# Kernel optimization log

Measured on AMD Instinct MI355X. Metric: run time of the kernel, lower is better.

## Reference

```python
import jax, jax.numpy as jnp
import numpy as np

K = 2  # shift stride from module init


def setup_inputs() -> dict:
    key = jax.random.key(0)
    k1, k2, k3 = jax.random.split(key, 3)
    # x: [B, C, D, H, W] dense volumetric features
    x = jax.random.normal(k1, (2, 128, 48, 48, 48), dtype=jnp.float32)
    # 1x1x1 Conv3d weight [out_channels, 2*in_channels] (kernel dims squeezed) + bias
    W = jax.random.normal(k2, (128, 256), dtype=jnp.float32) * 0.02
    b = jax.random.normal(k3, (128,), dtype=jnp.float32) * 0.02
    return {"x": x, "W": W, "b": b}


def _max_relative(x):
    # torch.cat([x[..., -i:], x[..., :-i]], dim=ax) == roll by +i along ax
    B, C, D, H, Wd = x.shape
    xj = jnp.zeros_like(x)  # x - x
    for axis, n in ((2, D), (3, H), (4, Wd)):
        for i in range(K, n, K):  # static shift schedule, fine under jit
            xj = jnp.maximum(xj, x - jnp.roll(x, i, axis=axis))
    return xj


def reference(x, W, b):
    xj = _max_relative(x)
    y = jnp.concatenate([x, xj], axis=1)  # [B, 2C, D, H, W]
    # 1x1x1 conv == channel GEMM
    out = jnp.einsum('bcdhw,oc->bodhw', y, W) + b[None, :, None, None, None]
    return jax.nn.relu(out)
```

## Files before the change

### kernel.cpp

```cpp
#include <hip/hip_runtime.h>
#include <hip/hip_bf16.h>

#define SVOL 110592
#define HD   2304
#define NDIM 48

typedef __attribute__((ext_vector_type(4))) float f32x4;
typedef __attribute__((ext_vector_type(8))) short bf16x8;
typedef __attribute__((ext_vector_type(2))) unsigned int u32x2;
typedef unsigned short ushort_t;
typedef unsigned int uint_t;

__global__ __launch_bounds__(256) void wconv_kernel(const float* __restrict__ W,
                                                    ushort_t* __restrict__ Wb) {
    int i = blockIdx.x * 256 + threadIdx.x;
    float f = W[i];
    __hip_bfloat16 h = __float2bfloat16(f);
    Wb[i] = *(ushort_t*)&h;
}

__global__ __launch_bounds__(256) void tables_kernel(const float* __restrict__ x,
                                                     float* __restrict__ tabDp,
                                                     float* __restrict__ tabH,
                                                     float* __restrict__ tabW) {
    __shared__ __align__(16) float sl[4 * HD];
    const int bc   = blockIdx.x;
    const int part = blockIdx.y;
    const float* __restrict__ xp = x + (size_t)bc * SVOL + (size_t)part * 16 * HD;
    const int t    = threadIdx.x;
    const int w4   = t >> 6;
    const int lane = t & 63;
    const int dlh  = t / NDIM;
    const int wh   = t - dlh * NDIM;

    f32x4 accD[3][2];
    #pragma unroll
    for (int s = 0; s < 3; ++s)
        #pragma unroll
        for (int p = 0; p < 2; ++p)
            #pragma unroll
            for (int e = 0; e < 4; ++e) accD[s][p][e] = 3e38f;

    for (int q = 0; q < 4; ++q) {
        const float* __restrict__ qp = xp + (size_t)q * 4 * HD;
        #pragma unroll
        for (int k = 0; k < 9; ++k) {
            const int i16 = (k * 4 + w4) * 64 + lane;
            __builtin_amdgcn_global_load_lds(
                (const __attribute__((address_space(1))) void*)(qp + (size_t)i16 * 4),
                (__attribute__((address_space(3))) void*)&sl[(k * 4 + w4) * 256],
                16, 0, 0);
        }
        __syncthreads();

        #pragma unroll
        for (int s = 0; s < 3; ++s) {
            const int j = t + s * 256;
            if (j < 576) {
                #pragma unroll
                for (int dl = 0; dl < 4; ++dl) {
                    f32x4 v = ((const f32x4*)sl)[dl * 576 + j];
                    #pragma unroll
                    for (int e = 0; e < 4; ++e)
                        accD[s][dl & 1][e] = fminf(accD[s][dl & 1][e], v[e]);
                }
            }
        }
        if (t < 192) {
            const int d = part * 16 + q * 4 + dlh;
            {
                const float* pb = sl + dlh * HD + wh;
                float m0 = 3e38f, m1 = 3e38f;
                #pragma unroll
                for (int h = 0; h < NDIM; h += 2) {
                    m0 = fminf(m0, pb[h * NDIM]);
                    m1 = fminf(m1, pb[(h + 1) * NDIM]);
                }
                tabH[(size_t)bc * 2 * HD + d * NDIM + wh]      = m0;
                tabH[(size_t)bc * 2 * HD + HD + d * NDIM + wh] = m1;
            }
            {
                const f32x4* pr = (const f32x4*)(sl + dlh * HD + wh * NDIM);
                const int rot = wh % 12;
                float m0 = 3e38f, m1 = 3e38f;
                #pragma unroll
                for (int j = 0; j < 12; ++j) {
                    int jj = j + rot; if (jj >= 12) jj -= 12;
                    f32x4 v = pr[jj];
                    m0 = fminf(m0, fminf(v[0], v[2]));
                    m1 = fminf(m1, fminf(v[1], v[3]));
                }
                tabW[(size_t)bc * 2 * HD + d * NDIM + wh]      = m0;
                tabW[(size_t)bc * 2 * HD + HD + d * NDIM + wh] = m1;
            }
        }
        __syncthreads();
    }

    float* tDo = tabDp + ((size_t)part * 256 + bc) * 2 * HD;
    #pragma unroll
    for (int s = 0; s < 3; ++s) {
        const int j = t + s * 256;
        if (j < 576) {
            *((f32x4*)(tDo + j * 4))      = accD[s][0];
            *((f32x4*)(tDo + HD + j * 4)) = accD[s][1];
        }
    }
}

__global__ __launch_bounds__(256) void elem_kernel(const float* __restrict__ x,
                                                   const float* __restrict__ tabDp,
                                                   const float* __restrict__ tabH,
                                                   const float* __restrict__ tabW,
                                                   ushort_t* __restrict__ ybf) {
    __shared__ __align__(16) float sD[2 * HD];
    __shared__ __align__(16) float sH[2 * 384];
    __shared__ __align__(16) float sW[2 * 384];
    const int slab = blockIdx.x;
    const int bc   = blockIdx.y;
    const int t    = threadIdx.x;
    const int b = bc >> 7, c = bc & 127;

    const float* tD0 = tabDp + ((size_t)0 * 256 + bc) * 2 * HD;
    const float* tD1 = tabDp + ((size_t)1 * 256 + bc) * 2 * HD;
    const float* tD2 = tabDp + ((size_t)2 * 256 + bc) * 2 * HD;
    for (int i = t; i < 2 * HD / 4; i += 256) {
        f32x4 a = ((const f32x4*)tD0)[i];
        f32x4 d1 = ((const f32x4*)tD1)[i];
        f32x4 d2 = ((const f32x4*)tD2)[i];
        f32x4 m;
        #pragma unroll
        for (int j = 0; j < 4; ++j) m[j] = fminf(a[j], fminf(d1[j], d2[j]));
        ((f32x4*)sD)[i] = m;
    }
    const float* tH = tabH + (size_t)bc * 2 * HD;
    const float* tW = tabW + (size_t)bc * 2 * HD;
    for (int i = t; i < 96; i += 256) {
        ((f32x4*)sH)[i]      = ((const f32x4*)(tH + slab * 384))[i];
        ((f32x4*)sH)[96 + i] = ((const f32x4*)(tH + HD + slab * 384))[i];
        ((f32x4*)sW)[i]      = ((const f32x4*)(tW + slab * 384))[i];
        ((f32x4*)sW)[96 + i] = ((const f32x4*)(tW + HD + slab * 384))[i];
    }
    __syncthreads();

    const float* __restrict__ xp = x + (size_t)bc * SVOL + (size_t)slab * 8 * HD;
    ushort_t* yx = ybf + (size_t)(b * 256 + c) * SVOL + (size_t)slab * 8 * HD;
    ushort_t* yj = yx + (size_t)128 * SVOL;

    for (int i4 = t; i4 < 8 * HD / 4; i4 += 256) {
        const int s = i4 * 4;
        const int dl = s / HD;
        const int r  = s - dl * HD;
        const int h  = r / NDIM;
        const int w0 = r - h * NDIM;
        const int pd = dl & 1, ph = h & 1;

        f32x4 v  = *(const f32x4*)(xp + s);
        f32x4 mD = *(const f32x4*)(sD + pd * HD + r);
        f32x4 mH = *(const f32x4*)(sH + ph * 384 + dl * NDIM + w0);
        const float mW0 = sW[dl * NDIM + h];
        const float mW1 = sW[384 + dl * NDIM + h];

        union { __hip_bfloat16 h4[4]; uint2 u; } ox, oj;
        #pragma unroll
        for (int j = 0; j < 4; ++j) {
            const float mm  = fminf(mD[j], fminf(mH[j], (j & 1) ? mW1 : mW0));
            const float xjv = fmaxf(0.0f, v[j] - mm);
            ox.h4[j] = __float2bfloat16(v[j]);
            oj.h4[j] = __float2bfloat16(xjv);
        }
        *(uint2*)(yx + s) = ox.u;
        *(uint2*)(yj + s) = oj.u;
    }
}

#define TPB 4
__global__ __launch_bounds__(256, 2) void gemm_kernel(const ushort_t* __restrict__ ybf,
                                                      const ushort_t* __restrict__ Wb,
                                                      const float* __restrict__ bias,
                                                      float* __restrict__ out) {
    __shared__ __align__(1024) ushort_t ytile[2][16384];
    const int tile0 = blockIdx.x * TPB;
    const int b  = blockIdx.y;
    const int t  = threadIdx.x;
    const int wid = t >> 6, lane = t & 63;
    const ushort_t* __restrict__ yb = ybf + (size_t)b * 256 * SVOL;

    const int wm = wid;
    const int l15 = lane & 15, l4 = lane >> 4;

    const ushort_t* wp = Wb + (size_t)(wm * 32 + l15) * 256 + l4 * 8;
    bf16x8 aw[2][8];
    #pragma unroll
    for (int m = 0; m < 2; ++m)
        #pragma unroll
        for (int kk = 0; kk < 8; ++kk)
            aw[m][kk] = *(const bf16x8*)(wp + ((size_t)m * 16 * 256 + kk * 32));
    float bv[2];
    #pragma unroll
    for (int m = 0; m < 2; ++m) bv[m] = bias[wm * 32 + m * 16 + l15];

    const int g    = lane >> 5;
    const int l5   = lane & 31;
    const int sq   = l5 >> 3;
    const int row  = (l5 >> 1) & 3;
    const int colh = l5 & 1;

#define STAGE(buf, tile)                                                              \
    {                                                                                 \
        const int s0_ = (tile) * 64;                                                  \
        _Pragma("unroll")                                                             \
        for (int it = 0; it < 8; ++it) {                                              \
            const int cq0 = (it * 4 + wid) * 2;                                       \
            const int c   = (cq0 + g) * 4 + row;                                      \
            const ushort_t* src = yb + (size_t)c * SVOL + (s0_ + sq * 16 + colh * 8); \
            __builtin_amdgcn_global_load_lds(                                         \
                (const __attribute__((address_space(1))) void*)src,                   \
                (__attribute__((address_space(3))) void*)&ytile[buf][cq0 * 256],      \
                16, 0, 0);                                                            \
        }                                                                             \
    }

    const uint_t lds_base = (uint_t)(uintptr_t)(__attribute__((address_space(3))) ushort_t*)&ytile[0][0];
    const uint_t addr0 = lds_base + (uint_t)(l4 * 1024 + l15 * 8);
    float* ob = out + (size_t)b * 128 * SVOL;

    STAGE(0, tile0)

    #pragma unroll
    for (int tt = 0; tt < TPB; ++tt) {
        __builtin_amdgcn_s_barrier();
        if (tt + 1 < TPB) STAGE((tt + 1) & 1, tile0 + tt + 1)
        __builtin_amdgcn_sched_barrier(0);
        if (tt == 0 || tt + 1 == TPB) asm volatile("s_waitcnt vmcnt(8)" ::: "memory");
        else                          asm volatile("s_waitcnt vmcnt(16)" ::: "memory");
        __builtin_amdgcn_sched_barrier(0);
        __builtin_amdgcn_s_barrier();

        const uint_t addrB = addr0 + (uint_t)((tt & 1) * 32768);
        f32x4 acc[4][2] = {};
        #pragma unroll
        for (int ph = 0; ph < 2; ++ph) {
            u32x2 lo[4][4], hi[4][4];
            #pragma unroll
            for (int kk = 0; kk < 4; ++kk)
                #pragma unroll
                for (int n = 0; n < 4; ++n) {
                    const uint_t ad = addrB + (uint_t)((ph * 4 + kk) * 4096 + n * 128);
                    asm volatile("ds_read_b64_tr_b16 %0, %2 offset:0\n\t"
                                 "ds_read_b64_tr_b16 %1, %2 offset:512"
                                 : "=&v"(lo[kk][n]), "=&v"(hi[kk][n]) : "v"(ad) : "memory");
                }
            asm volatile("s_waitcnt lgkmcnt(0)" ::: "memory");
            __builtin_amdgcn_sched_barrier(0);
            #pragma unroll
            for (int kk = 0; kk < 4; ++kk)
                #pragma unroll
                for (int n = 0; n < 4; ++n) {
                    union { u32x2 u2[2]; bf16x8 v; } cvt;
                    cvt.u2[0] = lo[kk][n]; cvt.u2[1] = hi[kk][n];
                    #pragma unroll
                    for (int m = 0; m < 2; ++m)
                        acc[n][m] = __builtin_amdgcn_mfma_f32_16x16x32_bf16(cvt.v, aw[m][ph * 4 + kk], acc[n][m], 0, 0, 0);
                }
        }

        const int s_b = (tile0 + tt) * 64;
        #pragma unroll
        for (int n = 0; n < 4; ++n)
            #pragma unroll
            for (int m = 0; m < 2; ++m) {
                const int o = wm * 32 + m * 16 + l15;
                const int s = s_b + n * 16 + l4 * 4;
                f32x4 r;
                #pragma unroll
                for (int j = 0; j < 4; ++j) r[j] = fmaxf(acc[n][m][j] + bv[m], 0.0f);
                *(f32x4*)(ob + (size_t)o * SVOL + s) = r;
            }
    }
#undef STAGE
}

extern "C" void kernel_launch(void* const* d_in, const int* in_sizes, int n_in,
                              void* d_out, int out_size, void* d_ws, size_t ws_size,
                              hipStream_t stream) {
    const float* x    = (const float*)d_in[0];
    const float* W    = (const float*)d_in[1];
    const float* bias = (const float*)d_in[2];
    float* out = (float*)d_out;

    ushort_t* ybf = (ushort_t*)d_ws;
    ushort_t* Wb  = (ushort_t*)((char*)d_ws + (size_t)2 * 256 * SVOL * 2);

    float* tabDp = (float*)d_out;
    float* tabH  = tabDp + (size_t)3 * 256 * 2 * HD;
    float* tabW  = tabH  + (size_t)256 * 2 * HD;

    wconv_kernel<<<128, 256, 0, stream>>>(W, Wb);
    tables_kernel<<<dim3(256, 3), 256, 0, stream>>>(x, tabDp, tabH, tabW);
    elem_kernel<<<dim3(6, 256), 256, 0, stream>>>(x, tabDp, tabH, tabW, ybf);
    gemm_kernel<<<dim3(SVOL / 64 / TPB, 2), 256, 0, stream>>>(ybf, Wb, bias, out);
}
```

Baseline: 137.4 us.

## Fuse elementwise relative-max construction into GEMM staging, drop bf16 intermediate

Removes the elem_kernel, which wrote a full bf16 copy of the concatenated [x, xj] tensor to global memory, and instead computes x and xj per tile inside the GEMM, packing them into registers and storing to LDS. A small merge kernel collapses the three partial D tables into one so the GEMM reads a single table. Weights are now reloaded from global memory per k-step instead of kept resident in registers, which frees registers but adds global/L2 traffic. The async global-to-LDS pipeline is replaced with register prefetch plus two __syncthreads per tile, which may expose more load latency.

```diff
diff --git a/kernel.cpp b/kernel.cpp
--- a/kernel.cpp
+++ b/kernel.cpp
@@ -108,74 +108,23 @@
     }
 }
 
-__global__ __launch_bounds__(256) void elem_kernel(const float* __restrict__ x,
-                                                   const float* __restrict__ tabDp,
-                                                   const float* __restrict__ tabH,
-                                                   const float* __restrict__ tabW,
-                                                   ushort_t* __restrict__ ybf) {
-    __shared__ __align__(16) float sD[2 * HD];
-    __shared__ __align__(16) float sH[2 * 384];
-    __shared__ __align__(16) float sW[2 * 384];
-    const int slab = blockIdx.x;
-    const int bc   = blockIdx.y;
-    const int t    = threadIdx.x;
-    const int b = bc >> 7, c = bc & 127;
-
-    const float* tD0 = tabDp + ((size_t)0 * 256 + bc) * 2 * HD;
-    const float* tD1 = tabDp + ((size_t)1 * 256 + bc) * 2 * HD;
-    const float* tD2 = tabDp + ((size_t)2 * 256 + bc) * 2 * HD;
-    for (int i = t; i < 2 * HD / 4; i += 256) {
-        f32x4 a = ((const f32x4*)tD0)[i];
-        f32x4 d1 = ((const f32x4*)tD1)[i];
-        f32x4 d2 = ((const f32x4*)tD2)[i];
-        f32x4 m;
-        #pragma unroll
-        for (int j = 0; j < 4; ++j) m[j] = fminf(a[j], fminf(d1[j], d2[j]));
-        ((f32x4*)sD)[i] = m;
-    }
-    const float* tH = tabH + (size_t)bc * 2 * HD;
-    const float* tW = tabW + (size_t)bc * 2 * HD;
-    for (int i = t; i < 96; i += 256) {
-        ((f32x4*)sH)[i]      = ((const f32x4*)(tH + slab * 384))[i];
-        ((f32x4*)sH)[96 + i] = ((const f32x4*)(tH + HD + slab * 384))[i];
-        ((f32x4*)sW)[i]      = ((const f32x4*)(tW + slab * 384))[i];
-        ((f32x4*)sW)[96 + i] = ((const f32x4*)(tW + HD + slab * 384))[i];
-    }
-    __syncthreads();
-
-    const float* __restrict__ xp = x + (size_t)bc * SVOL + (size_t)slab * 8 * HD;
-    ushort_t* yx = ybf + (size_t)(b * 256 + c) * SVOL + (size_t)slab * 8 * HD;
-    ushort_t* yj = yx + (size_t)128 * SVOL;
-
-    for (int i4 = t; i4 < 8 * HD / 4; i4 += 256) {
-        const int s = i4 * 4;
-        const int dl = s / HD;
-        const int r  = s - dl * HD;
-        const int h  = r / NDIM;
-        const int w0 = r - h * NDIM;
-        const int pd = dl & 1, ph = h & 1;
-
-        f32x4 v  = *(const f32x4*)(xp + s);
-        f32x4 mD = *(const f32x4*)(sD + pd * HD + r);
-        f32x4 mH = *(const f32x4*)(sH + ph * 384 + dl * NDIM + w0);
-        const float mW0 = sW[dl * NDIM + h];
-        const float mW1 = sW[384 + dl * NDIM + h];
-
-        union { __hip_bfloat16 h4[4]; uint2 u; } ox, oj;
-        #pragma unroll
-        for (int j = 0; j < 4; ++j) {
-            const float mm  = fminf(mD[j], fminf(mH[j], (j & 1) ? mW1 : mW0));
-            const float xjv = fmaxf(0.0f, v[j] - mm);
-            ox.h4[j] = __float2bfloat16(v[j]);
-            oj.h4[j] = __float2bfloat16(xjv);
-        }
-        *(uint2*)(yx + s) = ox.u;
-        *(uint2*)(yj + s) = oj.u;
-    }
+__global__ __launch_bounds__(256) void merge_kernel(const float* __restrict__ tabDp,
+                                                    float* __restrict__ tabD) {
+    const int i = blockIdx.x * 256 + threadIdx.x;
+    f32x4 a  = ((const f32x4*)tabDp)[i];
+    f32x4 d1 = ((const f32x4*)(tabDp + (size_t)256 * 2 * HD))[i];
+    f32x4 d2 = ((const f32x4*)(tabDp + (size_t)2 * 256 * 2 * HD))[i];
+    f32x4 m;
+    #pragma unroll
+    for (int j = 0; j < 4; ++j) m[j] = fminf(a[j], fminf(d1[j], d2[j]));
+    ((f32x4*)tabD)[i] = m;
 }
 
 #define TPB 4
-__global__ __launch_bounds__(256, 2) void gemm_kernel(const ushort_t* __restrict__ ybf,
+__global__ __launch_bounds__(256, 2) void gemm_kernel(const float* __restrict__ x,
+                                                      const float* __restrict__ tabD,
+                                                      const float* __restrict__ tabH,
+                                                      const float* __restrict__ tabW,
                                                       const ushort_t* __restrict__ Wb,
                                                       const float* __restrict__ bias,
                                                       float* __restrict__ out) {
@@ -184,69 +133,82 @@
     const int b  = blockIdx.y;
     const int t  = threadIdx.x;
     const int wid = t >> 6, lane = t & 63;
-    const ushort_t* __restrict__ yb = ybf + (size_t)b * 256 * SVOL;
-
-    const int wm = wid;
+    const int row  = lane & 3;
+    const int colq = (lane >> 2) & 3;
+    const int sqq  = (lane >> 4) & 3;
+    const int sloc = (sqq * 4 + colq) * 4;
     const int l15 = lane & 15, l4 = lane >> 4;
 
-    const ushort_t* wp = Wb + (size_t)(wm * 32 + l15) * 256 + l4 * 8;
-    bf16x8 aw[2][8];
-    #pragma unroll
-    for (int m = 0; m < 2; ++m)
-        #pragma unroll
-        for (int kk = 0; kk < 8; ++kk)
-            aw[m][kk] = *(const bf16x8*)(wp + ((size_t)m * 16 * 256 + kk * 32));
+    const float* __restrict__ xb = x + (size_t)b * 128 * SVOL;
+    const size_t tbb = (size_t)b * 128 * 2 * HD;
+
+    const ushort_t* wp = Wb + (size_t)(wid * 32 + l15) * 256 + l4 * 8;
     float bv[2];
     #pragma unroll
-    for (int m = 0; m < 2; ++m) bv[m] = bias[wm * 32 + m * 16 + l15];
-
-    const int g    = lane >> 5;
-    const int l5   = lane & 31;
-    const int sq   = l5 >> 3;
-    const int row  = (l5 >> 1) & 3;
-    const int colh = l5 & 1;
-
-#define STAGE(buf, tile)                                                              \
-    {                                                                                 \
-        const int s0_ = (tile) * 64;                                                  \
-        _Pragma("unroll")                                                             \
-        for (int it = 0; it < 8; ++it) {                                              \
-            const int cq0 = (it * 4 + wid) * 2;                                       \
-            const int c   = (cq0 + g) * 4 + row;                                      \
-            const ushort_t* src = yb + (size_t)c * SVOL + (s0_ + sq * 16 + colh * 8); \
-            __builtin_amdgcn_global_load_lds(                                         \
-                (const __attribute__((address_space(1))) void*)src,                   \
-                (__attribute__((address_space(3))) void*)&ytile[buf][cq0 * 256],      \
-                16, 0, 0);                                                            \
-        }                                                                             \
-    }
+    for (int m = 0; m < 2; ++m) bv[m] = bias[wid * 32 + m * 16 + l15];
+
+    const int d  = (tile0 * 64) / HD;
+    const int rb = tile0 * 64 - d * HD;
+    const int pd = d & 1;
+
+    uint2 pk[8][2];
+    auto stage = [&](int tile) {
+        const int r  = rb + (tile - tile0) * 64 + sloc;
+        const int h  = r / NDIM;
+        const int w0 = r - h * NDIM;
+        const int ph = h & 1;
+        const int s  = d * HD + r;
+        #pragma unroll
+        for (int it = 0; it < 8; ++it) {
+            const int c = (it * 4 + wid) * 4 + row;
+            const size_t tb = tbb + (size_t)c * 2 * HD;
+            f32x4 xv = *(const f32x4*)(xb + (size_t)c * SVOL + s);
+            f32x4 mD = *(const f32x4*)(tabD + tb + pd * HD + r);
+            f32x4 mH = *(const f32x4*)(tabH + tb + ph * HD + d * NDIM + w0);
+            const float mW0 = tabW[tb + d * NDIM + h];
+            const float mW1 = tabW[tb + HD + d * NDIM + h];
+            union { __hip_bfloat16 h4[4]; uint2 u; } ox, oj;
+            #pragma unroll
+            for (int j = 0; j < 4; ++j) {
+                const float mm = fminf(mD[j], fminf(mH[j], (j & 1) ? mW1 : mW0));
+                ox.h4[j] = __float2bfloat16(xv[j]);
+                oj.h4[j] = __float2bfloat16(fmaxf(0.0f, xv[j] - mm));
+            }
+            pk[it][0] = ox.u; pk[it][1] = oj.u;
+        }
+    };
 
     const uint_t lds_base = (uint_t)(uintptr_t)(__attribute__((address_space(3))) ushort_t*)&ytile[0][0];
-    const uint_t addr0 = lds_base + (uint_t)(l4 * 1024 + l15 * 8);
     float* ob = out + (size_t)b * 128 * SVOL;
 
-    STAGE(0, tile0)
+    stage(tile0);
 
     #pragma unroll
     for (int tt = 0; tt < TPB; ++tt) {
-        __builtin_amdgcn_s_barrier();
-        if (tt + 1 < TPB) STAGE((tt + 1) & 1, tile0 + tt + 1)
-        __builtin_amdgcn_sched_barrier(0);
-        if (tt == 0 || tt + 1 == TPB) asm volatile("s_waitcnt vmcnt(8)" ::: "memory");
-        else                          asm volatile("s_waitcnt vmcnt(16)" ::: "memory");
-        __builtin_amdgcn_sched_barrier(0);
-        __builtin_amdgcn_s_barrier();
-
-        const uint_t addrB = addr0 + (uint_t)((tt & 1) * 32768);
+        __syncthreads();
+        {
+            ushort_t* bufp = ytile[tt & 1];
+            #pragma unroll
+            for (int it = 0; it < 8; ++it) {
+                const int A = (it * 4 + wid) * 512 + sqq * 128 + row * 32 + colq * 8;
+                *(uint2*)&bufp[A >> 1]             = pk[it][0];
+                *(uint2*)&bufp[(A + 16384) >> 1]   = pk[it][1];
+            }
+        }
+        __syncthreads();
+
+        if (tt + 1 < TPB) stage(tile0 + tt + 1);
+
+        const uint_t addrB = lds_base + (uint_t)((tt & 1) * 32768 + l4 * 1024 + l15 * 8);
         f32x4 acc[4][2] = {};
         #pragma unroll
-        for (int ph = 0; ph < 2; ++ph) {
+        for (int ph2 = 0; ph2 < 2; ++ph2) {
             u32x2 lo[4][4], hi[4][4];
             #pragma unroll
             for (int kk = 0; kk < 4; ++kk)
                 #pragma unroll
                 for (int n = 0; n < 4; ++n) {
-                    const uint_t ad = addrB + (uint_t)((ph * 4 + kk) * 4096 + n * 128);
+                    const uint_t ad = addrB + (uint_t)((ph2 * 4 + kk) * 4096 + n * 128);
                     asm volatile("ds_read_b64_tr_b16 %0, %2 offset:0\n\t"
                                  "ds_read_b64_tr_b16 %1, %2 offset:512"
                                  : "=&v"(lo[kk][n]), "=&v"(hi[kk][n]) : "v"(ad) : "memory");
@@ -254,15 +216,20 @@
             asm volatile("s_waitcnt lgkmcnt(0)" ::: "memory");
             __builtin_amdgcn_sched_barrier(0);
             #pragma unroll
-            for (int kk = 0; kk < 4; ++kk)
+            for (int kk = 0; kk < 4; ++kk) {
+                bf16x8 aw[2];
+                #pragma unroll
+                for (int m = 0; m < 2; ++m)
+                    aw[m] = *(const bf16x8*)(wp + ((size_t)m * 16 * 256 + (ph2 * 4 + kk) * 32));
                 #pragma unroll
                 for (int n = 0; n < 4; ++n) {
                     union { u32x2 u2[2]; bf16x8 v; } cvt;
                     cvt.u2[0] = lo[kk][n]; cvt.u2[1] = hi[kk][n];
                     #pragma unroll
                     for (int m = 0; m < 2; ++m)
-                        acc[n][m] = __builtin_amdgcn_mfma_f32_16x16x32_bf16(cvt.v, aw[m][ph * 4 + kk], acc[n][m], 0, 0, 0);
-                }
+                        acc[n][m] = __builtin_amdgcn_mfma_f32_16x16x32_bf16(cvt.v, aw[m], acc[n][m], 0, 0, 0);
+                }
+            }
         }
 
         const int s_b = (tile0 + tt) * 64;
@@ -270,7 +237,7 @@
         for (int n = 0; n < 4; ++n)
             #pragma unroll
             for (int m = 0; m < 2; ++m) {
-                const int o = wm * 32 + m * 16 + l15;
+                const int o = wid * 32 + m * 16 + l15;
                 const int s = s_b + n * 16 + l4 * 4;
                 f32x4 r;
                 #pragma unroll
@@ -278,7 +245,6 @@
                 *(f32x4*)(ob + (size_t)o * SVOL + s) = r;
             }
     }
-#undef STAGE
 }
 
 extern "C" void kernel_launch(void* const* d_in, const int* in_sizes, int n_in,
@@ -289,15 +255,14 @@
     const float* bias = (const float*)d_in[2];
     float* out = (float*)d_out;
 
-    ushort_t* ybf = (ushort_t*)d_ws;
-    ushort_t* Wb  = (ushort_t*)((char*)d_ws + (size_t)2 * 256 * SVOL * 2);
-
-    float* tabDp = (float*)d_out;
+    ushort_t* Wb   = (ushort_t*)d_ws;
+    float* tabDp = (float*)((char*)d_ws + 65536);
     float* tabH  = tabDp + (size_t)3 * 256 * 2 * HD;
     float* tabW  = tabH  + (size_t)256 * 2 * HD;
+    float* tabD  = tabW  + (size_t)256 * 2 * HD;
 
     wconv_kernel<<<128, 256, 0, stream>>>(W, Wb);
     tables_kernel<<<dim3(256, 3), 256, 0, stream>>>(x, tabDp, tabH, tabW);
-    elem_kernel<<<dim3(6, 256), 256, 0, stream>>>(x, tabDp, tabH, tabW, ybf);
-    gemm_kernel<<<dim3(SVOL / 64 / TPB, 2), 256, 0, stream>>>(ybf, Wb, bias, out);
-}
+    merge_kernel<<<1152, 256, 0, stream>>>(tabDp, tabD);
+    gemm_kernel<<<dim3(SVOL / 64 / TPB, 2), 256, 0, stream>>>(x, tabD, tabH, tabW, Wb, bias, out);
+}
```

Result: slower. 193.9 us (+41.2%).
